# Kernel optimization log

Hardware: AMD Instinct MI355X
Metric: run time of the kernel (lower is better)

Reference implementation:

```python
import jax, jax.numpy as jnp
import numpy as np

VOCAB = 50000
EMB = 100
HID = 128
NPROD = 10000
PEMB = 50
B, T = 256, 512
IN = EMB + PEMB  # 150


def setup_inputs() -> dict:
    key = jax.random.key(0)
    ks = jax.random.split(key, 10)
    s = 1.0 / np.sqrt(HID)  # torch LSTM init scale
    emb = jax.random.normal(ks[0], (VOCAB, EMB), jnp.float32)
    emb = emb.at[0].set(0.0)  # padding_idx=0
    return {
        "review": jax.random.randint(ks[1], (B, T), 0, VOCAB),
        "product": jax.random.randint(ks[2], (B,), 0, NPROD),
        "embedding": emb,
        "product_embedding": jax.random.normal(ks[3], (NPROD, PEMB), jnp.float32),
        "W_ih": jax.random.uniform(ks[4], (4 * HID, IN), jnp.float32, -s, s),
        "W_hh": jax.random.uniform(ks[5], (4 * HID, HID), jnp.float32, -s, s),
        "b_ih": jax.random.uniform(ks[6], (4 * HID,), jnp.float32, -s, s),
        "b_hh": jax.random.uniform(ks[7], (4 * HID,), jnp.float32, -s, s),
        "fc_w": jax.random.uniform(ks[8], (1, HID), jnp.float32, -s, s),
        "fc_b": jax.random.uniform(ks[9], (1,), jnp.float32, -s, s),
    }


def _lstm_last_h(x_proj, W_hh):
    # x_proj: [T, B, 4H] = precomputed input projection + biases
    def step(carry, xg):
        h, c = carry
        gates = xg + h @ W_hh.T  # [B, 4H]
        i, f, g, o = jnp.split(gates, 4, axis=-1)  # torch gate order i,f,g,o
        i, f, o = jax.nn.sigmoid(i), jax.nn.sigmoid(f), jax.nn.sigmoid(o)
        g = jnp.tanh(g)
        c = f * c + i * g
        h = o * jnp.tanh(c)
        return (h, c), None

    b = x_proj.shape[1]
    init = (jnp.zeros((b, HID), x_proj.dtype), jnp.zeros((b, HID), x_proj.dtype))
    (h, _), _ = jax.lax.scan(step, init, x_proj)
    return h  # [B, H] — hidden state at last timestep


def reference(review, product, embedding, product_embedding, W_ih, W_hh, b_ih, b_hh, fc_w, fc_b):
    er = embedding[review]                       # [B, T, EMB]
    ep = product_embedding[product][:, None, :]  # [B, 1, PEMB]
    ep = jnp.broadcast_to(ep, (er.shape[0], er.shape[1], PEMB))
    combined = jnp.concatenate([er, ep], axis=-1)  # [B, T, IN]
    # precompute input projection for all timesteps in one GEMM
    x_proj = jnp.einsum('btd,gd->tbg', combined, W_ih) + (b_ih + b_hh)  # [T, B, 4H]
    h_last = _lstm_last_h(x_proj, W_hh)
    out = h_last @ fc_w.T + fc_b  # [B, 1]
    return jax.nn.sigmoid(out)
```

## Files before the change

### kernel.cpp

```cpp
#include <hip/hip_runtime.h>
#include <hip/hip_bf16.h>
#include <math.h>

#define VOCAB 50000
#define EMB 100
#define HID 128
#define NPROD 10000
#define PEMB 50
#define BSZ 256
#define TLEN 512
#define INDIM 150
#define G4 512

__device__ __forceinline__ int hpos(int k) { return k + ((k >> 5) << 2); }
#define HPAD 144

__global__ void k_transpose(const float* __restrict__ W_ih, float* __restrict__ Wt) {
    int idx = blockIdx.x * blockDim.x + threadIdx.x;
    if (idx < INDIM * G4) {
        int d = idx / G4, g = idx % G4;
        Wt[idx] = W_ih[g * INDIM + d];
    }
}

__global__ void k_pbias(const int* __restrict__ product,
                        const float* __restrict__ pemb,
                        const float* __restrict__ Wt,
                        const float* __restrict__ b_ih,
                        const float* __restrict__ b_hh,
                        float* __restrict__ pbias) {
    __shared__ float ep_s[PEMB];
    int b = blockIdx.x;
    int tid = threadIdx.x;
    int p = product[b];
    if (tid < PEMB) ep_s[tid] = pemb[p * PEMB + tid];
    __syncthreads();
    int g0 = tid, g1 = tid + 256;
    float a0 = b_ih[g0] + b_hh[g0];
    float a1 = b_ih[g1] + b_hh[g1];
    #pragma unroll 5
    for (int d = 0; d < PEMB; ++d) {
        float e = ep_s[d];
        a0 += e * Wt[(EMB + d) * G4 + g0];
        a1 += e * Wt[(EMB + d) * G4 + g1];
    }
    pbias[b * G4 + g0] = a0;
    pbias[b * G4 + g1] = a1;
}

__global__ void k_table(const float* __restrict__ emb,
                        const float* __restrict__ Wt,
                        float* __restrict__ table) {
    __shared__ __align__(16) float es[16 * EMB];
    int v0 = blockIdx.x * 16;
    int tid = threadIdx.x;
    for (int l = tid; l < 16 * EMB; l += 256) es[l] = emb[v0 * EMB + l];
    __syncthreads();
    float acc0[16], acc1[16];
    #pragma unroll
    for (int r = 0; r < 16; ++r) { acc0[r] = 0.f; acc1[r] = 0.f; }
    #pragma unroll 5
    for (int k4 = 0; k4 < EMB / 4; ++k4) {
        float w0[4], w1[4];
        #pragma unroll
        for (int j = 0; j < 4; ++j) {
            w0[j] = Wt[(k4 * 4 + j) * G4 + tid];
            w1[j] = Wt[(k4 * 4 + j) * G4 + tid + 256];
        }
        #pragma unroll
        for (int r = 0; r < 16; ++r) {
            float4 e = *reinterpret_cast<const float4*>(&es[r * EMB + k4 * 4]);
            acc0[r] += e.x * w0[0] + e.y * w0[1] + e.z * w0[2] + e.w * w0[3];
            acc1[r] += e.x * w1[0] + e.y * w1[1] + e.z * w1[2] + e.w * w1[3];
        }
    }
    #pragma unroll
    for (int r = 0; r < 16; ++r) {
        table[(v0 + r) * G4 + tid]       = acc0[r];
        table[(v0 + r) * G4 + tid + 256] = acc1[r];
    }
}

__global__ __launch_bounds__(512, 2) void k_lstm(
    const int* __restrict__ review,
    const float* __restrict__ W_hh,
    const float* __restrict__ table,
    const float* __restrict__ pbias,
    const float* __restrict__ fc_w,
    const float* __restrict__ fc_b,
    float* __restrict__ out) {
    __shared__ __align__(16) float hbuf[2][HPAD];
    __shared__ int rv_s[TLEN];
    int b = blockIdx.x;
    int tid = threadIdx.x;
    int u = tid >> 2;
    int q = tid & 3;

    rv_s[tid] = review[b * TLEN + tid];
    if (tid < HPAD) { hbuf[0][tid] = 0.f; hbuf[1][tid] = 0.f; }

    float4 w[4][8];
    #pragma unroll
    for (int gb = 0; gb < 4; ++gb) {
        const float* row = W_hh + (gb * HID + u) * HID + q * 32;
        #pragma unroll
        for (int j = 0; j < 8; ++j)
            w[gb][j] = *reinterpret_cast<const float4*>(row + j * 4);
    }

    float c = 0.f;
    float xi = 0, xf = 0, xg = 0, xo = 0;
    float ni = 0, nf = 0, ng = 0, no = 0;
    float pbi = 0, pbf = 0, pbg = 0, pbo = 0;
    __syncthreads();

    if (q == 0) {
        const float* trow = table + rv_s[0] * G4;
        ni = trow[u]; nf = trow[HID + u]; ng = trow[2 * HID + u]; no = trow[3 * HID + u];
        const float* pb = pbias + b * G4;
        pbi = pb[u]; pbf = pb[HID + u]; pbg = pb[2 * HID + u]; pbo = pb[3 * HID + u];
    }

    int p = 0;
    for (int t = 0; t < TLEN; ++t) {
        int vnext = rv_s[(t + 1) & (TLEN - 1)];
        if (q == 0) {
            xi = ni; xf = nf; xg = ng; xo = no;
            const float* trow = table + vnext * G4;
            ni = trow[u]; nf = trow[HID + u]; ng = trow[2 * HID + u]; no = trow[3 * HID + u];
        }
        float ai = 0, af = 0, ag = 0, ao = 0;
        #pragma unroll
        for (int j = 0; j < 8; ++j) {
            float4 h4 = *reinterpret_cast<const float4*>(&hbuf[p][q * 36 + j * 4]);
            ai += h4.x * w[0][j].x + h4.y * w[0][j].y + h4.z * w[0][j].z + h4.w * w[0][j].w;
            af += h4.x * w[1][j].x + h4.y * w[1][j].y + h4.z * w[1][j].z + h4.w * w[1][j].w;
            ag += h4.x * w[2][j].x + h4.y * w[2][j].y + h4.z * w[2][j].z + h4.w * w[2][j].w;
            ao += h4.x * w[3][j].x + h4.y * w[3][j].y + h4.z * w[3][j].z + h4.w * w[3][j].w;
        }
        ai += __shfl_xor(ai, 1); ai += __shfl_xor(ai, 2);
        af += __shfl_xor(af, 1); af += __shfl_xor(af, 2);
        ag += __shfl_xor(ag, 1); ag += __shfl_xor(ag, 2);
        ao += __shfl_xor(ao, 1); ao += __shfl_xor(ao, 2);
        if (q == 0) {
            float gi = 1.f / (1.f + expf(-(xi + pbi + ai)));
            float gf = 1.f / (1.f + expf(-(xf + pbf + af)));
            float gg = tanhf(xg + pbg + ag);
            float go = 1.f / (1.f + expf(-(xo + pbo + ao)));
            c = gf * c + gi * gg;
            float h = go * tanhf(c);
            hbuf[p ^ 1][hpos(u)] = h;
        }
        __syncthreads();
        p ^= 1;
    }
    if (tid < 64) {
        float v = hbuf[p][hpos(tid)] * fc_w[tid] + hbuf[p][hpos(tid + 64)] * fc_w[tid + 64];
        #pragma unroll
        for (int off = 32; off >= 1; off >>= 1) v += __shfl_xor(v, off);
        if (tid == 0) out[b] = 1.f / (1.f + expf(-(v + fc_b[0])));
    }
}

extern "C" void kernel_launch(void* const* d_in, const int* in_sizes, int n_in,
                              void* d_out, int out_size, void* d_ws, size_t ws_size,
                              hipStream_t stream) {
    const int*   review  = (const int*)d_in[0];
    const int*   product = (const int*)d_in[1];
    const float* emb     = (const float*)d_in[2];
    const float* pemb    = (const float*)d_in[3];
    const float* W_ih    = (const float*)d_in[4];
    const float* W_hh    = (const float*)d_in[5];
    const float* b_ih    = (const float*)d_in[6];
    const float* b_hh    = (const float*)d_in[7];
    const float* fc_w    = (const float*)d_in[8];
    const float* fc_b    = (const float*)d_in[9];
    float* out = (float*)d_out;

    char* ws = (char*)d_ws;
    float* Wt    = (float*)(ws);
    float* pbias = (float*)(ws + 307200);
    float* table = (float*)(ws + 831488);

    k_transpose<<<(INDIM * G4 + 255) / 256, 256, 0, stream>>>(W_ih, Wt);
    k_pbias<<<BSZ, 256, 0, stream>>>(product, pemb, Wt, b_ih, b_hh, pbias);
    k_table<<<VOCAB / 16, 256, 0, stream>>>(emb, Wt, table);
    k_lstm<<<BSZ, 512, 0, stream>>>(review, W_hh, table, pbias, fc_w, fc_b, out);
}
```

Before: 795.2 us.

## Map one thread per gate row in LSTM step and use fast activations

Each of the 512 threads now owns a full W_hh row (128 floats) in registers and computes one gate dot product without cross-lane shuffles. Activations are applied by all threads in parallel and exchanged through shared memory before the cell update. This replaces the old scheme of four lanes per unit with a shuffle reduction and a single-lane serial activation path. It also switches to __expf/rcp-based sigmoid and tanh. The cost is two barriers per timestep instead of one, much higher register pressure against launch_bounds(512,2), broadcast LDS reads, and reduced accuracy in the activations.

```diff
diff --git a/kernel.cpp b/kernel.cpp
--- a/kernel.cpp
+++ b/kernel.cpp
@@ -12,8 +12,16 @@
 #define INDIM 150
 #define G4 512
 
-__device__ __forceinline__ int hpos(int k) { return k + ((k >> 5) << 2); }
-#define HPAD 144
+typedef __attribute__((ext_vector_type(4))) float f32x4;
+
+__device__ __forceinline__ float sigm(float x) {
+    return __builtin_amdgcn_rcpf(1.f + __expf(-x));
+}
+__device__ __forceinline__ float tanh_fast(float x) {
+    float e = __expf(-2.f * fabsf(x));
+    float r = (1.f - e) * __builtin_amdgcn_rcpf(1.f + e);
+    return __builtin_copysignf(r, x);
+}
 
 __global__ void k_transpose(const float* __restrict__ W_ih, float* __restrict__ Wt) {
     int idx = blockIdx.x * blockDim.x + threadIdx.x;
@@ -89,76 +97,70 @@
     const float* __restrict__ fc_w,
     const float* __restrict__ fc_b,
     float* __restrict__ out) {
-    __shared__ __align__(16) float hbuf[2][HPAD];
+    __shared__ __align__(16) float hsA[HID];
+    __shared__ __align__(16) float hsB[HID];
+    __shared__ float gsh[G4];
     __shared__ int rv_s[TLEN];
     int b = blockIdx.x;
-    int tid = threadIdx.x;
-    int u = tid >> 2;
-    int q = tid & 3;
+    int g = threadIdx.x;
+    int wgate = g >> 7;
+    int u = g & 127;
 
-    rv_s[tid] = review[b * TLEN + tid];
-    if (tid < HPAD) { hbuf[0][tid] = 0.f; hbuf[1][tid] = 0.f; }
+    rv_s[g] = review[b * TLEN + g];
+    if (g < HID) { hsA[g] = 0.f; hsB[g] = 0.f; }
+    __syncthreads();
 
-    float4 w[4][8];
+    float x_cur = table[rv_s[0] * G4 + g];
+    float pb = pbias[b * G4 + g];
+
+    float w[128];
     #pragma unroll
-    for (int gb = 0; gb < 4; ++gb) {
-        const float* row = W_hh + (gb * HID + u) * HID + q * 32;
+    for (int j = 0; j < 32; ++j) {
+        f32x4 t = *reinterpret_cast<const f32x4*>(W_hh + g * HID + 4 * j);
+        w[4 * j + 0] = t.x; w[4 * j + 1] = t.y; w[4 * j + 2] = t.z; w[4 * j + 3] = t.w;
+    }
+    #pragma unroll
+    for (int k = 0; k < 128; ++k) asm volatile("" : "+v"(w[k]));
+
+    const float* hr = hsA;
+    float* hw = hsB;
+    float c = 0.f;
+
+    for (int t = 0; t < TLEN; ++t) {
+        float x_next = table[rv_s[(t + 1) & (TLEN - 1)] * G4 + g];
+
+        float a0 = 0.f, a1 = 0.f, a2 = 0.f, a3 = 0.f;
         #pragma unroll
-        for (int j = 0; j < 8; ++j)
-            w[gb][j] = *reinterpret_cast<const float4*>(row + j * 4);
+        for (int j = 0; j < 32; ++j) {
+            f32x4 h4 = *reinterpret_cast<const f32x4*>(&hr[4 * j]);
+            a0 += h4.x * w[4 * j + 0];
+            a1 += h4.y * w[4 * j + 1];
+            a2 += h4.z * w[4 * j + 2];
+            a3 += h4.w * w[4 * j + 3];
+        }
+        float pre = x_cur + pb + ((a0 + a1) + (a2 + a3));
+        float act = (wgate == 2) ? tanh_fast(pre) : sigm(pre);
+        gsh[g] = act;
+        __syncthreads();
+
+        float gi = gsh[u];
+        float gf = gsh[HID + u];
+        float gg = gsh[2 * HID + u];
+        float go = gsh[3 * HID + u];
+        c = gf * c + gi * gg;
+        float h = go * tanh_fast(c);
+        if (g < HID) hw[g] = h;
+        __syncthreads();
+
+        const float* tmp = hr; hr = hw; hw = (float*)tmp;
+        x_cur = x_next;
     }
 
-    float c = 0.f;
-    float xi = 0, xf = 0, xg = 0, xo = 0;
-    float ni = 0, nf = 0, ng = 0, no = 0;
-    float pbi = 0, pbf = 0, pbg = 0, pbo = 0;
-    __syncthreads();
-
-    if (q == 0) {
-        const float* trow = table + rv_s[0] * G4;
-        ni = trow[u]; nf = trow[HID + u]; ng = trow[2 * HID + u]; no = trow[3 * HID + u];
-        const float* pb = pbias + b * G4;
-        pbi = pb[u]; pbf = pb[HID + u]; pbg = pb[2 * HID + u]; pbo = pb[3 * HID + u];
-    }
-
-    int p = 0;
-    for (int t = 0; t < TLEN; ++t) {
-        int vnext = rv_s[(t + 1) & (TLEN - 1)];
-        if (q == 0) {
-            xi = ni; xf = nf; xg = ng; xo = no;
-            const float* trow = table + vnext * G4;
-            ni = trow[u]; nf = trow[HID + u]; ng = trow[2 * HID + u]; no = trow[3 * HID + u];
-        }
-        float ai = 0, af = 0, ag = 0, ao = 0;
-        #pragma unroll
-        for (int j = 0; j < 8; ++j) {
-            float4 h4 = *reinterpret_cast<const float4*>(&hbuf[p][q * 36 + j * 4]);
-            ai += h4.x * w[0][j].x + h4.y * w[0][j].y + h4.z * w[0][j].z + h4.w * w[0][j].w;
-            af += h4.x * w[1][j].x + h4.y * w[1][j].y + h4.z * w[1][j].z + h4.w * w[1][j].w;
-            ag += h4.x * w[2][j].x + h4.y * w[2][j].y + h4.z * w[2][j].z + h4.w * w[2][j].w;
-            ao += h4.x * w[3][j].x + h4.y * w[3][j].y + h4.z * w[3][j].z + h4.w * w[3][j].w;
-        }
-        ai += __shfl_xor(ai, 1); ai += __shfl_xor(ai, 2);
-        af += __shfl_xor(af, 1); af += __shfl_xor(af, 2);
-        ag += __shfl_xor(ag, 1); ag += __shfl_xor(ag, 2);
-        ao += __shfl_xor(ao, 1); ao += __shfl_xor(ao, 2);
-        if (q == 0) {
-            float gi = 1.f / (1.f + expf(-(xi + pbi + ai)));
-            float gf = 1.f / (1.f + expf(-(xf + pbf + af)));
-            float gg = tanhf(xg + pbg + ag);
-            float go = 1.f / (1.f + expf(-(xo + pbo + ao)));
-            c = gf * c + gi * gg;
-            float h = go * tanhf(c);
-            hbuf[p ^ 1][hpos(u)] = h;
-        }
-        __syncthreads();
-        p ^= 1;
-    }
-    if (tid < 64) {
-        float v = hbuf[p][hpos(tid)] * fc_w[tid] + hbuf[p][hpos(tid + 64)] * fc_w[tid + 64];
+    if (g < 64) {
+        float v = hr[g] * fc_w[g] + hr[g + 64] * fc_w[g + 64];
         #pragma unroll
         for (int off = 32; off >= 1; off >>= 1) v += __shfl_xor(v, off);
-        if (tid == 0) out[b] = 1.f / (1.f + expf(-(v + fc_b[0])));
+        if (g == 0) out[b] = sigm(v + fc_b[0]);
     }
 }
 
```

After: 653.3 us. 17.8% less time.
